# Performance work log

Measured on AMD Instinct MI355X. Metric: run time of the kernel, lower is better.

## Reference

```python
import jax, jax.numpy as jnp
import numpy as np

B, L, D = 2, 2048, 2048
H, KV, HD = 16, 4, 128          # num_heads, num_kv_heads, head_dim
RD = HD // 2                    # rope_dim = 64
G = H // KV                     # GQA groups


def _rotate_half(t):
    t1, t2 = jnp.split(t, 2, axis=-1)
    return jnp.concatenate([-t2, t1], axis=-1)


def setup_inputs() -> dict:
    key = jax.random.key(0)
    ks = jax.random.split(key, 8)
    x = jax.random.normal(ks[0], (B, L, D), dtype=jnp.float32)
    # proper RoPE cos/sin tables of width RD (half-rotation layout)
    inv_freq = 1.0 / (10000.0 ** (np.arange(0, RD, 2, dtype=np.float32) / RD))
    pos = np.arange(L, dtype=np.float32)
    freqs = np.outer(pos, inv_freq)               # [L, RD/2]
    emb = np.concatenate([freqs, freqs], axis=-1)  # [L, RD]
    cos = jnp.broadcast_to(jnp.cos(emb)[None], (B, L, RD)).astype(jnp.float32)
    sin = jnp.broadcast_to(jnp.sin(emb)[None], (B, L, RD)).astype(jnp.float32)
    s = 0.02
    Wq = jax.random.normal(ks[1], (H * HD, D), dtype=jnp.float32) * s
    bq = jnp.zeros((H * HD,), dtype=jnp.float32)
    Wkv = jax.random.normal(ks[2], (KV * HD, D), dtype=jnp.float32) * s
    bkv = jnp.zeros((KV * HD,), dtype=jnp.float32)
    Wrk = jax.random.normal(ks[3], (RD, D), dtype=jnp.float32) * s
    brk = jnp.zeros((RD,), dtype=jnp.float32)
    Wo = jax.random.normal(ks[4], (D, H * HD), dtype=jnp.float32) * s
    bo = jnp.zeros((D,), dtype=jnp.float32)
    return {"x": x, "cos": cos, "sin": sin, "Wq": Wq, "bq": bq,
            "Wkv": Wkv, "bkv": bkv, "Wrk": Wrk, "brk": brk, "Wo": Wo, "bo": bo}


def reference(x, cos, sin, Wq, bq, Wkv, bkv, Wrk, brk, Wo, bo):
    Bx, Lx, _ = x.shape
    q = (x @ Wq.T + bq).reshape(Bx, Lx, H, HD)            # [B,L,H,HD]
    kv = (x @ Wkv.T + bkv).reshape(Bx, Lx, KV, HD)        # [B,L,KV,HD]
    q_nope, q_rope = q[..., : HD - RD], q[..., HD - RD:]  # [.,HD-RD],[.,RD]
    k_rope = (x @ Wrk.T + brk).reshape(Bx, Lx, 1, RD)     # [B,L,1,RD]
    c = cos[:, :, None, :]
    s = sin[:, :, None, :]
    q_rope = q_rope * c + _rotate_half(q_rope) * s
    k_rope = k_rope * c + _rotate_half(k_rope) * s
    k_rope = jnp.broadcast_to(k_rope, (Bx, Lx, KV, RD))   # tied across kv heads
    q_states = jnp.concatenate([q_nope, q_rope], axis=-1)  # [B,L,H,HD]
    kv_tied = kv[..., : HD - RD]
    k_states = jnp.concatenate([kv_tied, k_rope], axis=-1)  # [B,L,KV,HD]
    v_states = kv                                            # cat(kv_tied, tail) == kv
    # GQA causal attention, scale 1/sqrt(HD)
    qg = q_states.reshape(Bx, Lx, KV, G, HD)
    scale = 1.0 / jnp.sqrt(jnp.asarray(HD, dtype=x.dtype))
    scores = jnp.einsum('bqkgd,bskd->bkgqs', qg, k_states) * scale
    mask = jnp.tril(jnp.ones((Lx, Lx), dtype=bool))
    scores = jnp.where(mask[None, None, None], scores, jnp.finfo(scores.dtype).min)
    probs = jax.nn.softmax(scores, axis=-1)
    out = jnp.einsum('bkgqs,bskd->bqkgd', probs, v_states)
    out = out.reshape(Bx, Lx, H * HD)
    return out @ Wo.T + bo
```

## Files before the change

kernel.cpp:

```cpp
#include <hip/hip_runtime.h>
#include <hip/hip_bf16.h>

#define BB   2
#define LL   2048
#define DD   2048
#define HH   16
#define KVH  4
#define HDD  128
#define RDD  64
#define MM   (BB*LL)

typedef __attribute__((ext_vector_type(4))) float f32x4;
typedef __attribute__((ext_vector_type(8))) short bf16x8;
typedef unsigned short u16;

static __device__ __forceinline__ u16 f2b(float f) {
  __hip_bfloat16 b = __float2bfloat16(f);
  return *(const u16*)&b;
}

static __device__ __forceinline__ void gload_lds16(const void* g, void* l) {
  __builtin_amdgcn_global_load_lds(
      (const __attribute__((address_space(1))) unsigned int*)g,
      (__attribute__((address_space(3))) unsigned int*)l, 16, 0, 0);
}

#define QSCALE 0.1275174313f

__global__ __launch_bounds__(256) void cast_bf16_kernel(const float* __restrict__ in,
                                                        u16* __restrict__ out, int n4) {
  int i = blockIdx.x * 256 + threadIdx.x;
  if (i >= n4) return;
  float4 v = ((const float4*)in)[i];
  ushort4 o;
  o.x = f2b(v.x); o.y = f2b(v.y); o.z = f2b(v.z); o.w = f2b(v.w);
  ((ushort4*)out)[i] = o;
}

__global__ __launch_bounds__(64) void gemm_bf16_nt(const u16* __restrict__ A,
                                                   const u16* __restrict__ W,
                                                   const float* __restrict__ bias,
                                                   float* __restrict__ C,
                                                   int M, int N, int K) {
  const int n0 = blockIdx.x * 16;
  const int m0 = blockIdx.y * 16;
  const int lane = threadIdx.x;
  const int r  = lane & 15;
  const int kq = (lane >> 4) * 8;
  const u16* ap = A + (size_t)(m0 + r) * K + kq;
  const u16* wp = W + (size_t)(n0 + r) * K + kq;
  f32x4 acc = {0.f, 0.f, 0.f, 0.f};
  for (int k = 0; k < K; k += 32) {
    bf16x8 a = *(const bf16x8*)(ap + k);
    bf16x8 b = *(const bf16x8*)(wp + k);
    acc = __builtin_amdgcn_mfma_f32_16x16x32_bf16(a, b, acc, 0, 0, 0);
  }
  const int col = lane & 15;
  const int rg  = (lane >> 4) * 4;
  const float bv = bias[n0 + col];
#pragma unroll
  for (int i = 0; i < 4; ++i)
    C[(size_t)(m0 + rg + i) * N + (n0 + col)] = acc[i] + bv;
}

__global__ __launch_bounds__(256) void gemm128(const u16* __restrict__ A,
                                               const u16* __restrict__ W,
                                               const float* __restrict__ bias,
                                               float* __restrict__ C,
                                               int M, int N, int K) {
  __shared__ u16 As[128 * 32];
  __shared__ u16 Bs[128 * 32];
  const int w = threadIdx.x >> 6, lane = threadIdx.x & 63;
  const int r = lane & 15, hi = lane >> 4, rg = hi * 4;
  const int wm = w >> 1, wn = w & 1;
  const int m0 = blockIdx.y * 128, n0 = blockIdx.x * 128;
  const int srow = w * 32 + (lane >> 2);
  const int scb  = (lane & 3) * 16;
  f32x4 acc[4][4];
#pragma unroll
  for (int i = 0; i < 4; ++i)
#pragma unroll
    for (int j = 0; j < 4; ++j) acc[i][j] = (f32x4){0.f, 0.f, 0.f, 0.f};

  for (int k0 = 0; k0 < K; k0 += 32) {
#pragma unroll
    for (int i = 0; i < 2; ++i) {
      gload_lds16((const char*)(A + (size_t)(m0 + srow + i * 16) * K + k0) + scb,
                  (char*)As + (w * 2 + i) * 1024);
      gload_lds16((const char*)(W + (size_t)(n0 + srow + i * 16) * K + k0) + scb,
                  (char*)Bs + (w * 2 + i) * 1024);
    }
    __syncthreads();
    bf16x8 a[4], b[4];
#pragma unroll
    for (int i = 0; i < 4; ++i)
      a[i] = *(const bf16x8*)((const char*)As + (wm * 64 + i * 16 + r) * 64 + hi * 16);
#pragma unroll
    for (int j = 0; j < 4; ++j)
      b[j] = *(const bf16x8*)((const char*)Bs + (wn * 64 + j * 16 + r) * 64 + hi * 16);
#pragma unroll
    for (int i = 0; i < 4; ++i)
#pragma unroll
      for (int j = 0; j < 4; ++j)
        acc[i][j] = __builtin_amdgcn_mfma_f32_16x16x32_bf16(a[i], b[j], acc[i][j], 0, 0, 0);
    __syncthreads();
  }
#pragma unroll
  for (int j = 0; j < 4; ++j) {
    const float bv = bias[n0 + wn * 64 + j * 16 + r];
#pragma unroll
    for (int i = 0; i < 4; ++i)
#pragma unroll
      for (int ii = 0; ii < 4; ++ii)
        C[(size_t)(m0 + wm * 64 + i * 16 + rg + ii) * N + n0 + wn * 64 + j * 16 + r] =
            acc[i][j][ii] + bv;
  }
}

__global__ __launch_bounds__(256) void gemm_q_fused(const u16* __restrict__ A,
                                                    const u16* __restrict__ W,
                                                    const float* __restrict__ bias,
                                                    const float* __restrict__ cosb,
                                                    const float* __restrict__ sinb,
                                                    u16* __restrict__ Qb) {
  __shared__ u16 As[128 * 32];
  __shared__ u16 Bs[128 * 32];
  const int w = threadIdx.x >> 6, lane = threadIdx.x & 63;
  const int r = lane & 15, hi = lane >> 4, rg = hi * 4;
  const int wm = w >> 1, wn = w & 1;
  const int h = blockIdx.x;
  const int m0 = blockIdx.y * 128, n0 = h * 128;
  const int srow = w * 32 + (lane >> 2);
  const int scb  = (lane & 3) * 16;
  f32x4 acc[4][4];
#pragma unroll
  for (int i = 0; i < 4; ++i)
#pragma unroll
    for (int j = 0; j < 4; ++j) acc[i][j] = (f32x4){0.f, 0.f, 0.f, 0.f};

  for (int k0 = 0; k0 < DD; k0 += 32) {
#pragma unroll
    for (int i = 0; i < 2; ++i) {
      gload_lds16((const char*)(A + (size_t)(m0 + srow + i * 16) * DD + k0) + scb,
                  (char*)As + (w * 2 + i) * 1024);
      gload_lds16((const char*)(W + (size_t)(n0 + srow + i * 16) * DD + k0) + scb,
                  (char*)Bs + (w * 2 + i) * 1024);
    }
    __syncthreads();
    bf16x8 a[4], b[4];
#pragma unroll
    for (int i = 0; i < 4; ++i)
      a[i] = *(const bf16x8*)((const char*)As + (wm * 64 + i * 16 + r) * 64 + hi * 16);
#pragma unroll
    for (int j = 0; j < 4; ++j)
      b[j] = *(const bf16x8*)((const char*)Bs + (wn * 64 + j * 16 + r) * 64 + hi * 16);
#pragma unroll
    for (int i = 0; i < 4; ++i)
#pragma unroll
      for (int j = 0; j < 4; ++j)
        acc[i][j] = __builtin_amdgcn_mfma_f32_16x16x32_bf16(a[i], b[j], acc[i][j], 0, 0, 0);
    __syncthreads();
  }

  const int b = m0 >> 11;
  const int lbase = (m0 & 2047) + wm * 64;
  u16* Qimg = Qb + (size_t)((b * 16 + h) * 128) * 2048;
  if (wn == 0) {
#pragma unroll
    for (int j = 0; j < 4; ++j) {
      const int d = j * 16 + r;
      const float bv = bias[h * 128 + d];
#pragma unroll
      for (int i = 0; i < 4; ++i)
#pragma unroll
        for (int ii = 0; ii < 4; ++ii) {
          const int l = lbase + i * 16 + rg + ii;
          Qimg[(size_t)(l >> 4) * 2048 + (d >> 5) * 512 + ((d >> 3) & 3) * 128 +
               (l & 15) * 8 + (d & 7)] = f2b((acc[i][j][ii] + bv) * QSCALE);
        }
    }
  } else {
#pragma unroll
    for (int jp = 0; jp < 2; ++jp) {
      const int dd0 = jp * 16 + r;
      const int dd1 = dd0 + 32;
      const float bv0 = bias[h * 128 + 64 + dd0];
      const float bv1 = bias[h * 128 + 64 + dd1];
#pragma unroll
      for (int i = 0; i < 4; ++i)
#pragma unroll
        for (int ii = 0; ii < 4; ++ii) {
          const int l = lbase + i * 16 + rg + ii;
          const size_t nb = (size_t)(b * 2048 + l) * 64;
          const float c0 = cosb[nb + dd0], s0 = sinb[nb + dd0];
          const float c1 = cosb[nb + dd1], s1 = sinb[nb + dd1];
          const float a0 = acc[i][jp][ii] + bv0;
          const float a1 = acc[i][jp + 2][ii] + bv1;
          const float v0 = (a0 * c0 - a1 * s0) * QSCALE;
          const float v1 = (a1 * c1 + a0 * s1) * QSCALE;
          const int d0f = 64 + dd0, d1f = 64 + dd1;
          const size_t rowoff = (size_t)(l >> 4) * 2048 + (l & 15) * 8;
          Qimg[rowoff + (d0f >> 5) * 512 + ((d0f >> 3) & 3) * 128 + (d0f & 7)] = f2b(v0);
          Qimg[rowoff + (d1f >> 5) * 512 + ((d1f >> 3) & 3) * 128 + (d1f & 7)] = f2b(v1);
        }
    }
  }
}

__global__ __launch_bounds__(256) void gemm_kv_fused(const u16* __restrict__ A,
                                                     const u16* __restrict__ W,
                                                     const float* __restrict__ bias,
                                                     u16* __restrict__ Kb,
                                                     u16* __restrict__ VTb) {
  __shared__ u16 As[128 * 32];
  __shared__ u16 Bs[128 * 32];
  const int w = threadIdx.x >> 6, lane = threadIdx.x & 63;
  const int r = lane & 15, hi = lane >> 4, rg = hi * 4;
  const int wm = w >> 1, wn = w & 1;
  const int c = blockIdx.x;
  const int m0 = blockIdx.y * 128, n0 = c * 128;
  const int srow = w * 32 + (lane >> 2);
  const int scb  = (lane & 3) * 16;
  f32x4 acc[4][4];
#pragma unroll
  for (int i = 0; i < 4; ++i)
#pragma unroll
    for (int j = 0; j < 4; ++j) acc[i][j] = (f32x4){0.f, 0.f, 0.f, 0.f};

  for (int k0 = 0; k0 < DD; k0 += 32) {
#pragma unroll
    for (int i = 0; i < 2; ++i) {
      gload_lds16((const char*)(A + (size_t)(m0 + srow + i * 16) * DD + k0) + scb,
                  (char*)As + (w * 2 + i) * 1024);
      gload_lds16((const char*)(W + (size_t)(n0 + srow + i * 16) * DD + k0) + scb,
                  (char*)Bs + (w * 2 + i) * 1024);
    }
    __syncthreads();
    bf16x8 a[4], b[4];
#pragma unroll
    for (int i = 0; i < 4; ++i)
      a[i] = *(const bf16x8*)((const char*)As + (wm * 64 + i * 16 + r) * 64 + hi * 16);
#pragma unroll
    for (int j = 0; j < 4; ++j)
      b[j] = *(const bf16x8*)((const char*)Bs + (wn * 64 + j * 16 + r) * 64 + hi * 16);
#pragma unroll
    for (int i = 0; i < 4; ++i)
#pragma unroll
      for (int j = 0; j < 4; ++j)
        acc[i][j] = __builtin_amdgcn_mfma_f32_16x16x32_bf16(a[i], b[j], acc[i][j], 0, 0, 0);
    __syncthreads();
  }

  const int b = m0 >> 11;
  const int lbase = (m0 & 2047) + wm * 64;
  u16* Kimg = Kb + (size_t)(b * KVH + c) * 32 * 8192;
  u16* Vimg = VTb + (size_t)(b * KVH + c) * 32 * 8192;
#pragma unroll
  for (int j = 0; j < 4; ++j) {
    const int d = wn * 64 + j * 16 + r;
    const float bv = bias[c * 128 + d];
#pragma unroll
    for (int i = 0; i < 4; ++i)
#pragma unroll
      for (int ii = 0; ii < 4; ++ii) {
        const int l = lbase + i * 16 + rg + ii;
        const u16 bf = f2b(acc[i][j][ii] + bv);
        const int lt = l & 63;
        Vimg[(size_t)(l >> 6) * 8192 + ((d >> 4) * 2 + ((lt >> 5) & 1)) * 512 +
             ((lt >> 2) & 3) * 128 + (d & 15) * 8 + ((lt >> 4) & 1) * 4 + (lt & 3)] = bf;
        if (wn == 0)
          Kimg[(size_t)(l >> 6) * 8192 + ((lt >> 4) & 3) * 2048 + (d >> 5) * 512 +
               ((d >> 3) & 3) * 128 + (lt & 15) * 8 + (d & 7)] = bf;
      }
  }
}

__global__ __launch_bounds__(256) void build_kr(const float* __restrict__ krbuf,
                                                const float* __restrict__ cosb,
                                                const float* __restrict__ sinb,
                                                u16* __restrict__ Kb) {
  const int tid = blockIdx.x * 256 + threadIdx.x;
  const int r   = tid & 15;
  const int hi  = (tid >> 4) & 3;
  const int ks2 = (tid >> 6) & 1;
  const int tt  = (tid >> 7) & 3;
  const int til = tid >> 9;
  const int stile = til & 31, bc = til >> 5;
  const int b = bc >> 2;
  const int s = stile * 64 + tt * 16 + r;
  const int n = b * LL + s;
  const int i0 = ks2 * 32 + hi * 8;
  const float* kr = krbuf + (size_t)n * RDD;
  const float* cb = cosb + (size_t)n * RDD + i0;
  const float* sb = sinb + (size_t)n * RDD + i0;
  float v[8];
  if (ks2 == 0) {
#pragma unroll
    for (int j = 0; j < 8; ++j) v[j] = kr[i0 + j] * cb[j] - kr[i0 + j + 32] * sb[j];
  } else {
#pragma unroll
    for (int j = 0; j < 8; ++j) v[j] = kr[i0 + j] * cb[j] + kr[i0 + j - 32] * sb[j];
  }
  u16 o[8];
#pragma unroll
  for (int j = 0; j < 8; ++j) o[j] = f2b(v[j]);
  u16* dst = Kb + (size_t)til * 8192 + tt * 2048 + (2 + ks2) * 512 + hi * 128 + r * 8;
  *(ushort4*)dst = *(ushort4*)&o[0];
  *(ushort4*)(dst + 4) = *(ushort4*)&o[4];
}

static __device__ __forceinline__ void stage_g(const u16* Kt, const u16* Vt,
                                               char* GB, int buf, int wg, int lane) {
#pragma unroll
  for (int i = 0; i < 4; ++i) {
    const int j = wg * 4 + i;
    gload_lds16(Kt + (size_t)j * 512 + lane * 8, (u16*)(GB + buf * 16384) + j * 512);
    gload_lds16(Vt + (size_t)j * 512 + lane * 8, (u16*)(GB + 32768 + buf * 16384) + j * 512);
  }
}

__global__ __launch_bounds__(512, 2) void attn_mfma10(const u16* __restrict__ Qb,
                                                      const u16* __restrict__ Kb,
                                                      const u16* __restrict__ VTb,
                                                      u16* __restrict__ attn_bf) {
  const int id = blockIdx.x;
  const int g = id & 31;
  const int s = id >> 5;
  const int bc = g & 7, hlow = g >> 3;
  const int b = bc >> 2, c = bc & 3;
  const int h = c * 4 + hlow;
  const int bh = b * 16 + h;
  const int w = threadIdx.x >> 6, lane = threadIdx.x & 63;
  const int r = lane & 15, hi = lane >> 4, rg = hi * 4;
  const int grp = w >> 2, wg = w & 3;

  __shared__ __align__(16) char LB[131072];
  char* GB = LB + grp * 65536;

  const u16* Ktg = Kb + (size_t)(b * KVH + c) * 32 * 8192;
  const u16* Vtg = VTb + (size_t)(b * KVH + c) * 32 * 8192;

  for (int ss = 0; ss < 2; ++ss) {
    const int qb = ss ? s : (15 - s);
    const int q0 = qb * 128 + wg * 32;
    const int half = qb + 1;
    const int tb = grp ? half : 0;

    bf16x8 qf[2][4];
#pragma unroll
    for (int qs = 0; qs < 2; ++qs) {
      const u16* qtb = Qb + (size_t)(bh * 128 + qb * 8 + wg * 2 + qs) * 2048;
#pragma unroll
      for (int ks = 0; ks < 4; ++ks)
        qf[qs][ks] = *(const bf16x8*)(qtb + ks * 512 + lane * 8);
    }

    float m_[2] = {-3.0e38f, -3.0e38f}, l_[2] = {0.f, 0.f};
    f32x4 o[2][8];
#pragma unroll
    for (int qs = 0; qs < 2; ++qs)
#pragma unroll
      for (int t = 0; t < 8; ++t) o[qs][t] = (f32x4){0.f, 0.f, 0.f, 0.f};

    stage_g(Ktg + (size_t)tb * 8192, Vtg + (size_t)tb * 8192, GB, 0, wg, lane);
    __syncthreads();
    int cur = 0;

    for (int t = 0; t < half; ++t) {
      if (t + 1 < half)
        stage_g(Ktg + (size_t)(tb + t + 1) * 8192, Vtg + (size_t)(tb + t + 1) * 8192,
                GB, cur ^ 1, wg, lane);
      const int s0 = (tb + t) * 64;

      if (s0 <= q0 + 31) {
        const u16* Kl = (const u16*)(GB + cur * 16384);
        const u16* Vl = (const u16*)(GB + 32768 + cur * 16384);

        f32x4 st[2][4];
#pragma unroll
        for (int qs = 0; qs < 2; ++qs)
#pragma unroll
          for (int tt = 0; tt < 4; ++tt) st[qs][tt] = (f32x4){0.f, 0.f, 0.f, 0.f};
        __builtin_amdgcn_s_setprio(1);
#pragma unroll
        for (int tt = 0; tt < 4; ++tt) {
          bf16x8 kf[4];
#pragma unroll
          for (int ks = 0; ks < 4; ++ks)
            kf[ks] = *(const bf16x8*)(Kl + tt * 2048 + ks * 512 + lane * 8);
#pragma unroll
          for (int qs = 0; qs < 2; ++qs)
#pragma unroll
            for (int ks = 0; ks < 4; ++ks)
              st[qs][tt] = __builtin_amdgcn_mfma_f32_16x16x32_bf16(kf[ks], qf[qs][ks], st[qs][tt], 0, 0, 0);
        }
        __builtin_amdgcn_s_setprio(0);

        if (s0 + 63 > q0) {
#pragma unroll
          for (int qs = 0; qs < 2; ++qs)
#pragma unroll
            for (int tt = 0; tt < 4; ++tt)
#pragma unroll
              for (int i = 0; i < 4; ++i)
                if (s0 + tt * 16 + rg + i > q0 + qs * 16 + r) st[qs][tt][i] = -3.0e38f;
        }

        float vmax[2];
#pragma unroll
        for (int qs = 0; qs < 2; ++qs) {
          float v = st[qs][0][0];
#pragma unroll
          for (int tt = 0; tt < 4; ++tt)
#pragma unroll
            for (int i = 0; i < 4; ++i) v = fmaxf(v, st[qs][tt][i]);
          v = fmaxf(v, __shfl_xor(v, 16));
          v = fmaxf(v, __shfl_xor(v, 32));
          vmax[qs] = v;
        }
        const float grow = fmaxf(vmax[0] - m_[0], vmax[1] - m_[1]);
        if (!__all(grow <= 11.54f)) {
#pragma unroll
          for (int qs = 0; qs < 2; ++qs) {
            const float mn = fmaxf(m_[qs], vmax[qs]);
            const float cf = exp2f(m_[qs] - mn);
            l_[qs] *= cf;
            m_[qs] = mn;
#pragma unroll
            for (int tt = 0; tt < 8; ++tt)
#pragma unroll
              for (int i = 0; i < 4; ++i) o[qs][tt][i] *= cf;
          }
        }
        bf16x8 pa[2][2];
#pragma unroll
        for (int qs = 0; qs < 2; ++qs) {
          float ps = 0.f;
#pragma unroll
          for (int tt = 0; tt < 4; ++tt)
#pragma unroll
            for (int i = 0; i < 4; ++i) {
              st[qs][tt][i] = exp2f(st[qs][tt][i] - m_[qs]);
              ps += st[qs][tt][i];
            }
          ps += __shfl_xor(ps, 16);
          ps += __shfl_xor(ps, 32);
          l_[qs] += ps;
#pragma unroll
          for (int kb = 0; kb < 2; ++kb) {
            bf16x8 v;
#pragma unroll
            for (int jj = 0; jj < 8; ++jj)
              v[jj] = (short)f2b(st[qs][2 * kb + (jj >> 2)][jj & 3]);
            pa[qs][kb] = v;
          }
        }

        __builtin_amdgcn_s_setprio(1);
#pragma unroll
        for (int tt = 0; tt < 8; ++tt) {
#pragma unroll
          for (int kb = 0; kb < 2; ++kb) {
            bf16x8 vf = *(const bf16x8*)(Vl + tt * 1024 + kb * 512 + lane * 8);
#pragma unroll
            for (int qs = 0; qs < 2; ++qs)
              o[qs][tt] = __builtin_amdgcn_mfma_f32_16x16x32_bf16(pa[qs][kb], vf, o[qs][tt], 0, 0, 0);
          }
        }
        __builtin_amdgcn_s_setprio(0);
      }

      __syncthreads();
      cur ^= 1;
    }

    float2* mlp = (float2*)(LB + 65536);
    if (hi == 0) {
      mlp[(w * 2 + 0) * 16 + r] = make_float2(m_[0], l_[0]);
      mlp[(w * 2 + 1) * 16 + r] = make_float2(m_[1], l_[1]);
    }
    __syncthreads();
    float lC[2], asc[2];
#pragma unroll
    for (int qs = 0; qs < 2; ++qs) {
      const float2 p = mlp[((w ^ 4) * 2 + qs) * 16 + r];
      const float mn = fmaxf(m_[qs], p.x);
      const float a1 = exp2f(m_[qs] - mn);
      lC[qs] = l_[qs] * a1 + p.y * exp2f(p.x - mn);
      asc[qs] = a1;
    }
#pragma unroll
    for (int qs = 0; qs < 2; ++qs) {
      float ai[4];
#pragma unroll
      for (int i = 0; i < 4; ++i) ai[i] = __shfl(asc[qs], (lane & 48) + rg + i);
#pragma unroll
      for (int tt = 0; tt < 8; ++tt)
#pragma unroll
        for (int i = 0; i < 4; ++i) o[qs][tt][i] *= ai[i];
    }
    if (grp == 1) {
#pragma unroll
      for (int qs = 0; qs < 2; ++qs)
#pragma unroll
        for (int tt = 0; tt < 8; ++tt)
          *(f32x4*)(LB + wg * 16384 + (qs * 8 + tt) * 1024 + lane * 16) = o[qs][tt];
    }
    __syncthreads();
    if (grp == 0) {
#pragma unroll
      for (int qs = 0; qs < 2; ++qs) {
#pragma unroll
        for (int tt = 0; tt < 8; ++tt)
          o[qs][tt] += *(const f32x4*)(LB + wg * 16384 + (qs * 8 + tt) * 1024 + lane * 16);
        const float il = 1.f / lC[qs];
        float inv[4];
#pragma unroll
        for (int i = 0; i < 4; ++i) inv[i] = __shfl(il, (lane & 48) + rg + i);
        u16* op = attn_bf + (size_t)(b * LL + q0 + qs * 16 + rg) * DD + h * HDD;
#pragma unroll
        for (int tt = 0; tt < 8; ++tt)
#pragma unroll
          for (int i = 0; i < 4; ++i)
            op[(size_t)i * DD + tt * 16 + r] = f2b(o[qs][tt][i] * inv[i]);
      }
    }
    __syncthreads();
  }
}

extern "C" void kernel_launch(void* const* d_in, const int* in_sizes, int n_in,
                              void* d_out, int out_size, void* d_ws, size_t ws_size,
                              hipStream_t stream) {
  const float* x    = (const float*)d_in[0];
  const float* cosb = (const float*)d_in[1];
  const float* sinb = (const float*)d_in[2];
  const float* Wq   = (const float*)d_in[3];
  const float* bq   = (const float*)d_in[4];
  const float* Wkv  = (const float*)d_in[5];
  const float* bkv  = (const float*)d_in[6];
  const float* Wrk  = (const float*)d_in[7];
  const float* brk  = (const float*)d_in[8];
  const float* Wo   = (const float*)d_in[9];
  const float* bo   = (const float*)d_in[10];
  float* out = (float*)d_out;

  char* ws = (char*)d_ws;
  u16*   Qb    = (u16*)(ws);
  u16*   attn_bf = (u16*)(ws + 16777216);
  u16*   xb    = (u16*)(ws + 33554432);
  u16*   Wqb   = (u16*)(ws + 50331648);
  u16*   Wob   = (u16*)(ws + 58720256);
  u16*   Wkvb  = (u16*)(ws + 67108864);
  u16*   Wrkb  = (u16*)(ws + 69206016);
  float* krbuf = (float*)(ws + 69468160);
  u16*   Kb    = (u16*)(ws + 70516736);
  u16*   VTb   = (u16*)(ws + 74711040);

  cast_bf16_kernel<<<(MM * DD / 4) / 256, 256, 0, stream>>>(x, xb, MM * DD / 4);
  cast_bf16_kernel<<<(HH * HDD * DD / 4) / 256, 256, 0, stream>>>(Wq, Wqb, HH * HDD * DD / 4);
  cast_bf16_kernel<<<(KVH * HDD * DD / 4) / 256, 256, 0, stream>>>(Wkv, Wkvb, KVH * HDD * DD / 4);
  cast_bf16_kernel<<<(RDD * DD / 4) / 256, 256, 0, stream>>>(Wrk, Wrkb, RDD * DD / 4);
  cast_bf16_kernel<<<(DD * HH * HDD / 4) / 256, 256, 0, stream>>>(Wo, Wob, DD * HH * HDD / 4);

  gemm_bf16_nt<<<dim3(RDD / 16, MM / 16), 64, 0, stream>>>(xb, Wrkb, brk, krbuf, MM, RDD, DD);

  gemm_q_fused<<<dim3(HH, MM / 128), 256, 0, stream>>>(xb, Wqb, bq, cosb, sinb, Qb);
  gemm_kv_fused<<<dim3(KVH, MM / 128), 256, 0, stream>>>(xb, Wkvb, bkv, Kb, VTb);
  build_kr<<<512, 256, 0, stream>>>(krbuf, cosb, sinb, Kb);

  attn_mfma10<<<dim3(256), 512, 0, stream>>>(Qb, Kb, VTb, attn_bf);

  gemm128<<<dim3(DD / 128, MM / 128), 256, 0, stream>>>(attn_bf, Wob, bo, out, MM, DD, DD);
}
```

Baseline: 248.7 us.

## Merge cast kernels and fuse rope-key GEMM with RoPE and K-image scatter

Replaces the five separate fp32-to-bf16 cast launches with a single kernel that picks its source buffer by index range. It also replaces the small rope-key GEMM and the separate build_kr pass with one fused kernel. That kernel splits K across four waves, reduces the partial sums in shared memory, applies bias and rotary embedding, and scatters bf16 results straight into the K tile images. This removes launch overhead and the fp32 krbuf round trip through memory, at the cost of scattered 2-byte stores and a shared-memory reduction.

New measurement: 231.5 us, median of 2. -6.9%, faster.

```diff
diff --git a/kernel.cpp b/kernel.cpp
--- a/kernel.cpp
+++ b/kernel.cpp
@@ -27,40 +27,25 @@
 
 #define QSCALE 0.1275174313f
 
-__global__ __launch_bounds__(256) void cast_bf16_kernel(const float* __restrict__ in,
-                                                        u16* __restrict__ out, int n4) {
-  int i = blockIdx.x * 256 + threadIdx.x;
-  if (i >= n4) return;
-  float4 v = ((const float4*)in)[i];
+__global__ __launch_bounds__(256) void cast_all(const float* __restrict__ x,
+                                                const float* __restrict__ Wq,
+                                                const float* __restrict__ Wkv,
+                                                const float* __restrict__ Wrk,
+                                                const float* __restrict__ Wo,
+                                                u16* __restrict__ xb, u16* __restrict__ Wqb,
+                                                u16* __restrict__ Wkvb, u16* __restrict__ Wrkb,
+                                                u16* __restrict__ Wob) {
+  const int i = blockIdx.x * 256 + threadIdx.x;
+  const float* src; u16* dst; int off;
+  if (i < 2097152)      { src = x;   dst = xb;   off = i; }
+  else if (i < 3145728) { src = Wq;  dst = Wqb;  off = i - 2097152; }
+  else if (i < 3407872) { src = Wkv; dst = Wkvb; off = i - 3145728; }
+  else if (i < 3440640) { src = Wrk; dst = Wrkb; off = i - 3407872; }
+  else                  { src = Wo;  dst = Wob;  off = i - 3440640; }
+  float4 v = ((const float4*)src)[off];
   ushort4 o;
   o.x = f2b(v.x); o.y = f2b(v.y); o.z = f2b(v.z); o.w = f2b(v.w);
-  ((ushort4*)out)[i] = o;
-}
-
-__global__ __launch_bounds__(64) void gemm_bf16_nt(const u16* __restrict__ A,
-                                                   const u16* __restrict__ W,
-                                                   const float* __restrict__ bias,
-                                                   float* __restrict__ C,
-                                                   int M, int N, int K) {
-  const int n0 = blockIdx.x * 16;
-  const int m0 = blockIdx.y * 16;
-  const int lane = threadIdx.x;
-  const int r  = lane & 15;
-  const int kq = (lane >> 4) * 8;
-  const u16* ap = A + (size_t)(m0 + r) * K + kq;
-  const u16* wp = W + (size_t)(n0 + r) * K + kq;
-  f32x4 acc = {0.f, 0.f, 0.f, 0.f};
-  for (int k = 0; k < K; k += 32) {
-    bf16x8 a = *(const bf16x8*)(ap + k);
-    bf16x8 b = *(const bf16x8*)(wp + k);
-    acc = __builtin_amdgcn_mfma_f32_16x16x32_bf16(a, b, acc, 0, 0, 0);
-  }
-  const int col = lane & 15;
-  const int rg  = (lane >> 4) * 4;
-  const float bv = bias[n0 + col];
-#pragma unroll
-  for (int i = 0; i < 4; ++i)
-    C[(size_t)(m0 + rg + i) * N + (n0 + col)] = acc[i] + bv;
+  ((ushort4*)dst)[off] = o;
 }
 
 __global__ __launch_bounds__(256) void gemm128(const u16* __restrict__ A,
@@ -275,38 +260,63 @@
   }
 }
 
-__global__ __launch_bounds__(256) void build_kr(const float* __restrict__ krbuf,
-                                                const float* __restrict__ cosb,
-                                                const float* __restrict__ sinb,
-                                                u16* __restrict__ Kb) {
-  const int tid = blockIdx.x * 256 + threadIdx.x;
-  const int r   = tid & 15;
-  const int hi  = (tid >> 4) & 3;
-  const int ks2 = (tid >> 6) & 1;
-  const int tt  = (tid >> 7) & 3;
-  const int til = tid >> 9;
-  const int stile = til & 31, bc = til >> 5;
-  const int b = bc >> 2;
-  const int s = stile * 64 + tt * 16 + r;
-  const int n = b * LL + s;
-  const int i0 = ks2 * 32 + hi * 8;
-  const float* kr = krbuf + (size_t)n * RDD;
-  const float* cb = cosb + (size_t)n * RDD + i0;
-  const float* sb = sinb + (size_t)n * RDD + i0;
-  float v[8];
-  if (ks2 == 0) {
-#pragma unroll
-    for (int j = 0; j < 8; ++j) v[j] = kr[i0 + j] * cb[j] - kr[i0 + j + 32] * sb[j];
-  } else {
-#pragma unroll
-    for (int j = 0; j < 8; ++j) v[j] = kr[i0 + j] * cb[j] + kr[i0 + j - 32] * sb[j];
-  }
-  u16 o[8];
-#pragma unroll
-  for (int j = 0; j < 8; ++j) o[j] = f2b(v[j]);
-  u16* dst = Kb + (size_t)til * 8192 + tt * 2048 + (2 + ks2) * 512 + hi * 128 + r * 8;
-  *(ushort4*)dst = *(ushort4*)&o[0];
-  *(ushort4*)(dst + 4) = *(ushort4*)&o[4];
+__global__ __launch_bounds__(256) void gemm_rk_fused(const u16* __restrict__ A,
+                                                     const u16* __restrict__ Wrkb,
+                                                     const float* __restrict__ brk,
+                                                     const float* __restrict__ cosb,
+                                                     const float* __restrict__ sinb,
+                                                     u16* __restrict__ Kb) {
+  __shared__ f32x4 red[4][2][64];
+  const int w = threadIdx.x >> 6, lane = threadIdx.x & 63;
+  const int bx = blockIdx.x;
+  const int m0 = blockIdx.y * 16;
+  const int r = lane & 15;
+  const int kq = (lane >> 4) * 8;
+  const u16* ap  = A + (size_t)(m0 + r) * DD + kq;
+  const u16* wp0 = Wrkb + (size_t)(bx * 16 + r) * DD + kq;
+  const u16* wp1 = Wrkb + (size_t)(bx * 16 + 32 + r) * DD + kq;
+  f32x4 acc0 = {0.f, 0.f, 0.f, 0.f}, acc1 = {0.f, 0.f, 0.f, 0.f};
+  for (int k = w * 512; k < w * 512 + 512; k += 32) {
+    bf16x8 a  = *(const bf16x8*)(ap + k);
+    bf16x8 b0 = *(const bf16x8*)(wp0 + k);
+    bf16x8 b1 = *(const bf16x8*)(wp1 + k);
+    acc0 = __builtin_amdgcn_mfma_f32_16x16x32_bf16(a, b0, acc0, 0, 0, 0);
+    acc1 = __builtin_amdgcn_mfma_f32_16x16x32_bf16(a, b1, acc1, 0, 0, 0);
+  }
+  red[w][0][lane] = acc0;
+  red[w][1][lane] = acc1;
+  __syncthreads();
+  if (w == 0) {
+#pragma unroll
+    for (int ww = 1; ww < 4; ++ww) {
+      acc0 += red[ww][0][lane];
+      acc1 += red[ww][1][lane];
+    }
+    const int rg = (lane >> 4) * 4;
+    const int dd0 = bx * 16 + r, dd1 = dd0 + 32;
+    const float bv0 = brk[dd0], bv1 = brk[dd1];
+    const int d0f = 64 + dd0, d1f = 64 + dd1;
+#pragma unroll
+    for (int i = 0; i < 4; ++i) {
+      const int n = m0 + rg + i;
+      const int b = n >> 11, l = n & 2047;
+      const size_t nb = (size_t)n * 64;
+      const float c0 = cosb[nb + dd0], s0 = sinb[nb + dd0];
+      const float c1 = cosb[nb + dd1], s1 = sinb[nb + dd1];
+      const float a0 = acc0[i] + bv0;
+      const float a1 = acc1[i] + bv1;
+      const u16 v0 = f2b(a0 * c0 - a1 * s0);
+      const u16 v1 = f2b(a1 * c1 + a0 * s1);
+      const int lt = l & 63;
+      const size_t loff = (size_t)(l >> 6) * 8192 + ((lt >> 4) & 3) * 2048 + (lt & 15) * 8;
+#pragma unroll
+      for (int c = 0; c < 4; ++c) {
+        u16* Kimg = Kb + (size_t)(b * KVH + c) * 32 * 8192;
+        Kimg[loff + (d0f >> 5) * 512 + ((d0f >> 3) & 3) * 128 + (d0f & 7)] = v0;
+        Kimg[loff + (d1f >> 5) * 512 + ((d1f >> 3) & 3) * 128 + (d1f & 7)] = v1;
+      }
+    }
+  }
 }
 
 static __device__ __forceinline__ void stage_g(const u16* Kt, const u16* Vt,
@@ -553,21 +563,14 @@
   u16*   Wob   = (u16*)(ws + 58720256);
   u16*   Wkvb  = (u16*)(ws + 67108864);
   u16*   Wrkb  = (u16*)(ws + 69206016);
-  float* krbuf = (float*)(ws + 69468160);
   u16*   Kb    = (u16*)(ws + 70516736);
   u16*   VTb   = (u16*)(ws + 74711040);
 
-  cast_bf16_kernel<<<(MM * DD / 4) / 256, 256, 0, stream>>>(x, xb, MM * DD / 4);
-  cast_bf16_kernel<<<(HH * HDD * DD / 4) / 256, 256, 0, stream>>>(Wq, Wqb, HH * HDD * DD / 4);
-  cast_bf16_kernel<<<(KVH * HDD * DD / 4) / 256, 256, 0, stream>>>(Wkv, Wkvb, KVH * HDD * DD / 4);
-  cast_bf16_kernel<<<(RDD * DD / 4) / 256, 256, 0, stream>>>(Wrk, Wrkb, RDD * DD / 4);
-  cast_bf16_kernel<<<(DD * HH * HDD / 4) / 256, 256, 0, stream>>>(Wo, Wob, DD * HH * HDD / 4);
-
-  gemm_bf16_nt<<<dim3(RDD / 16, MM / 16), 64, 0, stream>>>(xb, Wrkb, brk, krbuf, MM, RDD, DD);
+  cast_all<<<17536, 256, 0, stream>>>(x, Wq, Wkv, Wrk, Wo, xb, Wqb, Wkvb, Wrkb, Wob);
 
   gemm_q_fused<<<dim3(HH, MM / 128), 256, 0, stream>>>(xb, Wqb, bq, cosb, sinb, Qb);
   gemm_kv_fused<<<dim3(KVH, MM / 128), 256, 0, stream>>>(xb, Wkvb, bkv, Kb, VTb);
-  build_kr<<<512, 256, 0, stream>>>(krbuf, cosb, sinb, Kb);
+  gemm_rk_fused<<<dim3(2, MM / 16), 256, 0, stream>>>(xb, Wrkb, brk, cosb, sinb, Kb);
 
   attn_mfma10<<<dim3(256), 512, 0, stream>>>(Qb, Kb, VTb, attn_bf);
 
```
